# Kernel tuning notes

Hardware: AMD Instinct MI355X
Metric: run time of the kernel (lower is better)

## Reference

```python
import jax, jax.numpy as jnp
import numpy as np

NUM_HEADS = 16
HEAD_DIM = 64  # hidden 1024 / 16 heads


def setup_inputs() -> dict:
    key = jax.random.key(0)
    ks = jax.random.split(key, 4)
    B, S, D = 2, 2048, 1024
    scale = 1.0 / np.sqrt(D)
    return {
        "hidden_states": jax.random.normal(ks[0], (B, S, D), jnp.float32),
        "Wq": jax.random.normal(ks[1], (D, D), jnp.float32) * scale,
        "bq": jnp.zeros((D,), jnp.float32),
        "Wk": jax.random.normal(ks[2], (D, D), jnp.float32) * scale,
        "bk": jnp.zeros((D,), jnp.float32),
        "Wv": jax.random.normal(ks[3], (D, D), jnp.float32) * scale,
        "bv": jnp.zeros((D,), jnp.float32),
    }


def _split_heads(x):
    B, S, D = x.shape
    return x.reshape(B, S, NUM_HEADS, HEAD_DIM).transpose(0, 2, 1, 3)  # [B,H,S,dh]


def reference(hidden_states, Wq, bq, Wk, bk, Wv, bv):
    q = _split_heads(hidden_states @ Wq + bq)
    k = _split_heads(hidden_states @ Wk + bk)
    v = _split_heads(hidden_states @ Wv + bv)
    scores = jnp.einsum("bhqd,bhkd->bhqk", q, k) / jnp.sqrt(
        jnp.asarray(HEAD_DIM, hidden_states.dtype))
    probs = jax.nn.softmax(scores, axis=-1)  # dropout is identity in eval mode
    ctx = jnp.einsum("bhqk,bhkd->bhqd", probs, v)
    B, H, S, dh = ctx.shape
    return ctx.transpose(0, 2, 1, 3).reshape(B, S, H * dh)
```

## Files before the change

### kernel.cpp

```cpp
#include <hip/hip_runtime.h>
#include <hip/hip_bf16.h>


typedef __attribute__((ext_vector_type(8))) short bf16x8;
typedef __attribute__((ext_vector_type(4))) float f32x4;
typedef __attribute__((ext_vector_type(4))) int int4v;

#define MFMA16(A, B, C) __builtin_amdgcn_mfma_f32_16x16x32_bf16((A), (B), (C), 0, 0, 0)

#if __has_builtin(__builtin_amdgcn_exp2f)
#define EXP2(x) __builtin_amdgcn_exp2f(x)
#else
#define EXP2(x) exp2f(x)
#endif

static __device__ __forceinline__ unsigned short f2bf(float f) {
    union { float f; unsigned int u; } v;
    v.f = f;
    unsigned int u = v.u;
    u += ((u >> 16) & 1u) + 0x7FFFu;
    return (unsigned short)(u >> 16);
}

static __device__ __forceinline__ void gload_lds16(const void* g, void* l) {
    __builtin_amdgcn_global_load_lds(
        (const __attribute__((address_space(1))) void*)g,
        (__attribute__((address_space(3))) void*)l, 16, 0, 0);
}

__global__ __launch_bounds__(256) void cast_hs(const float* __restrict__ in,
                                               unsigned short* __restrict__ out) {
    const size_t i = ((size_t)blockIdx.x * 256 + threadIdx.x) * 8;
    float4 a0 = *reinterpret_cast<const float4*>(in + i);
    float4 a1 = *reinterpret_cast<const float4*>(in + i + 4);
    unsigned short t[8];
    t[0] = f2bf(a0.x); t[1] = f2bf(a0.y); t[2] = f2bf(a0.z); t[3] = f2bf(a0.w);
    t[4] = f2bf(a1.x); t[5] = f2bf(a1.y); t[6] = f2bf(a1.z); t[7] = f2bf(a1.w);
    *reinterpret_cast<int4v*>(out + i) = *reinterpret_cast<int4v*>(t);
}

__global__ __launch_bounds__(256) void transpose_cast_w(
    const float* __restrict__ W0, const float* __restrict__ W1,
    const float* __restrict__ W2, unsigned short* __restrict__ Wt) {
    __shared__ float Ts[64][65];
    const float* W = (blockIdx.z == 0) ? W0 : (blockIdx.z == 1) ? W1 : W2;
    unsigned short* O = Wt + (size_t)blockIdx.z * 1048576;

    const int t  = threadIdx.x;
    const int k0 = blockIdx.y * 64;
    const int n0 = blockIdx.x * 64;

    {
        const int kr = t >> 2, nc = (t & 3) * 16;
        const float* p = W + (size_t)(k0 + kr) * 1024 + n0 + nc;
        float4 r0 = *reinterpret_cast<const float4*>(p);
        float4 r1 = *reinterpret_cast<const float4*>(p + 4);
        float4 r2 = *reinterpret_cast<const float4*>(p + 8);
        float4 r3 = *reinterpret_cast<const float4*>(p + 12);
        float* d = &Ts[kr][nc];
        d[0]=r0.x; d[1]=r0.y; d[2]=r0.z; d[3]=r0.w;
        d[4]=r1.x; d[5]=r1.y; d[6]=r1.z; d[7]=r1.w;
        d[8]=r2.x; d[9]=r2.y; d[10]=r2.z; d[11]=r2.w;
        d[12]=r3.x; d[13]=r3.y; d[14]=r3.z; d[15]=r3.w;
    }
    __syncthreads();
    {
        const int nr = t >> 2, kc = (t & 3) * 16;
        unsigned short tmp[16];
#pragma unroll
        for (int i = 0; i < 16; i++) tmp[i] = f2bf(Ts[kc + i][nr]);
        unsigned short* d = O + (size_t)(n0 + nr) * 1024 + k0 + kc;
        *reinterpret_cast<int4v*>(d)     = *reinterpret_cast<int4v*>(&tmp[0]);
        *reinterpret_cast<int4v*>(d + 8) = *reinterpret_cast<int4v*>(&tmp[8]);
    }
}

__global__ __launch_bounds__(256) void qkv_gemm_dma(
    const unsigned short* __restrict__ hsb,
    const unsigned short* __restrict__ Wt,
    const float* __restrict__ b0, const float* __restrict__ b1,
    const float* __restrict__ b2,
    unsigned short* __restrict__ Qo,
    unsigned short* __restrict__ Ko,
    unsigned short* __restrict__ Vto)
{
    __shared__ unsigned short As[128][32];
    __shared__ unsigned short Bs[128][32];

    const int z = blockIdx.z;
    const unsigned short* W = Wt + (size_t)z * 1048576;
    const float* bias = (z == 0) ? b0 : (z == 1) ? b1 : b2;

    const int tid  = threadIdx.x;
    const int lane = tid & 63;
    const int w    = tid >> 6;
    const int l15  = lane & 15;
    const int quad = lane >> 4;
    const int m0   = blockIdx.y * 128;
    const int n0   = blockIdx.x * 128;
    const int wm   = (w >> 1) * 64;
    const int wn   = (w & 1) * 64;

    const int drow = lane >> 2;
    const int dcol = (lane & 3) * 8;

    f32x4 acc[4][4];
#pragma unroll
    for (int i = 0; i < 4; i++)
#pragma unroll
        for (int j = 0; j < 4; j++)
            acc[i][j] = (f32x4){0.f, 0.f, 0.f, 0.f};

    for (int k0 = 0; k0 < 1024; k0 += 32) {
        __syncthreads();
#pragma unroll
        for (int p = 0; p < 2; p++) {
            const int s = w * 2 + p;
            gload_lds16(hsb + (size_t)(m0 + s * 16 + drow) * 1024 + k0 + dcol,
                        &As[s * 16][0]);
            gload_lds16(W   + (size_t)(n0 + s * 16 + drow) * 1024 + k0 + dcol,
                        &Bs[s * 16][0]);
        }
        __syncthreads();

        bf16x8 af[4], bfr[4];
#pragma unroll
        for (int i = 0; i < 4; i++)
            af[i] = *reinterpret_cast<const bf16x8*>(&As[wm + i * 16 + l15][quad * 8]);
#pragma unroll
        for (int j = 0; j < 4; j++)
            bfr[j] = *reinterpret_cast<const bf16x8*>(&Bs[wn + j * 16 + l15][quad * 8]);
#pragma unroll
        for (int i = 0; i < 4; i++)
#pragma unroll
            for (int j = 0; j < 4; j++)
                acc[i][j] = MFMA16(af[i], bfr[j], acc[i][j]);
    }

    if (z == 0) {
        const float qs = 0.18033688f;
#pragma unroll
        for (int i = 0; i < 4; i++) {
            const int mbase = m0 + wm + i * 16 + quad * 4;
#pragma unroll
            for (int j = 0; j < 4; j++) {
                const int n = n0 + wn + j * 16 + l15;
                const int h = n >> 6, d = n & 63;
                const float bn = bias[n];
#pragma unroll
                for (int r = 0; r < 4; r++) {
                    const int mm = mbase + r;
                    const int b = mm >> 11, s = mm & 2047;
                    Qo[(((size_t)(b * 16 + h) * 2048 + s) * 64) + d] =
                        f2bf((acc[i][j][r] + bn) * qs);
                }
            }
        }
    } else if (z == 1) {
#pragma unroll
        for (int i = 0; i < 4; i++) {
            const int mbase = m0 + wm + i * 16 + quad * 4;
#pragma unroll
            for (int j = 0; j < 4; j++) {
                const int n = n0 + wn + j * 16 + l15;
                const int h = n >> 6, d = n & 63;
                const float bn = bias[n];
#pragma unroll
                for (int r = 0; r < 4; r++) {
                    const int mm = mbase + r;
                    const int b = mm >> 11, s = mm & 2047;
                    const int dsw = ((((d >> 3) ^ (s & 7)) & 7) << 3) | (d & 7);
                    Ko[(((size_t)(b * 16 + h) * 2048 + s) * 64) + dsw] =
                        f2bf(acc[i][j][r] + bn);
                }
            }
        }
    } else {
#pragma unroll
        for (int i = 0; i < 4; i++) {
            const int mbase = m0 + wm + i * 16 + quad * 4;
            const int b = mbase >> 11, s0 = mbase & 2047;
#pragma unroll
            for (int j = 0; j < 4; j++) {
                const int n = n0 + wn + j * 16 + l15;
                const int h = n >> 6, d = n & 63;
                const float bn = bias[n];
                ushort4 v4;
                v4.x = f2bf(acc[i][j][0] + bn);
                v4.y = f2bf(acc[i][j][1] + bn);
                v4.z = f2bf(acc[i][j][2] + bn);
                v4.w = f2bf(acc[i][j][3] + bn);
                const int cs  = (s0 & 63) >> 3;
                const int ssw = (s0 & ~63) | (((cs ^ (d & 7)) & 7) << 3) | (s0 & 7);
                *reinterpret_cast<ushort4*>(
                    Vto + ((size_t)(b * 16 + h) * 64 + d) * 2048 + ssw) = v4;
            }
        }
    }
}

__global__ __launch_bounds__(512) void attn3(
    const unsigned short* __restrict__ Qg,
    const unsigned short* __restrict__ Kg,
    const unsigned short* __restrict__ Vtg,
    float* __restrict__ out)
{
    __shared__ unsigned short Ks[2][64][64];
    __shared__ unsigned short Vs[2][64][64];
    __shared__ unsigned short Ps[8][16][66];

    const int tid  = threadIdx.x;
    const int lane = tid & 63;
    const int w    = tid >> 6;
    const int l15  = lane & 15;
    const int quad = lane >> 4;

    const int q0 = blockIdx.x * 128;
    const int h  = blockIdx.y;
    const int b  = blockIdx.z;
    const size_t base = (size_t)(b * 16 + h) * 2048 * 64;
    const unsigned short* Qh  = Qg  + base;
    const unsigned short* Kh  = Kg  + base;
    const unsigned short* Vth = Vtg + base;

    const int drow = lane >> 3;
    const int dcol = (lane & 7) * 8;

    bf16x8 qf[2];
#pragma unroll
    for (int ks = 0; ks < 2; ks++)
        qf[ks] = *reinterpret_cast<const bf16x8*>(
            Qh + (size_t)(q0 + w * 16 + l15) * 64 + ks * 32 + quad * 8);

    f32x4 o[4];
#pragma unroll
    for (int t = 0; t < 4; t++) o[t] = (f32x4){0.f, 0.f, 0.f, 0.f};
    float rsum[4] = {0.f, 0.f, 0.f, 0.f};

    const int c0 = (((quad + 0) ^ (l15 & 7)) & 7) * 8;
    const int c1 = (((quad + 4) ^ (l15 & 7)) & 7) * 8;

    gload_lds16(Kh  + (size_t)(w * 8 + drow) * 64 + dcol,   &Ks[0][w * 8][0]);
    gload_lds16(Vth + (size_t)(w * 8 + drow) * 2048 + dcol, &Vs[0][w * 8][0]);
    __syncthreads();

    int cur = 0;
    for (int kt = 0; kt < 32; kt++) {
        if (kt < 31) {
            const int kn = kt + 1;
            gload_lds16(Kh  + (size_t)kn * 4096 + (size_t)(w * 8 + drow) * 64 + dcol,
                        &Ks[cur ^ 1][w * 8][0]);
            gload_lds16(Vth + (size_t)(w * 8 + drow) * 2048 + kn * 64 + dcol,
                        &Vs[cur ^ 1][w * 8][0]);
        }

        const unsigned short (*Kc)[64] = Ks[cur];
        const unsigned short (*Vc)[64] = Vs[cur];

#pragma unroll
        for (int t = 0; t < 4; t++) {
            f32x4 sc = (f32x4){0.f, 0.f, 0.f, 0.f};
            {
                bf16x8 kf = *reinterpret_cast<const bf16x8*>(&Kc[t * 16 + l15][c0]);
                sc = MFMA16(qf[0], kf, sc);
            }
            {
                bf16x8 kf = *reinterpret_cast<const bf16x8*>(&Kc[t * 16 + l15][c1]);
                sc = MFMA16(qf[1], kf, sc);
            }
#pragma unroll
            for (int r = 0; r < 4; r++) {
                const float p = EXP2(sc[r]);
                rsum[r] += p;
                Ps[w][quad * 4 + r][t * 16 + l15] = f2bf(p);
            }
        }

        asm volatile("s_waitcnt lgkmcnt(0)" ::: "memory");
        __builtin_amdgcn_sched_barrier(0);

        bf16x8 pf[2];
#pragma unroll
        for (int ks = 0; ks < 2; ks++)
            pf[ks] = *reinterpret_cast<const bf16x8*>(&Ps[w][l15][ks * 32 + quad * 8]);

#pragma unroll
        for (int t = 0; t < 4; t++) {
            {
                bf16x8 vf = *reinterpret_cast<const bf16x8*>(&Vc[t * 16 + l15][c0]);
                o[t] = MFMA16(pf[0], vf, o[t]);
            }
            {
                bf16x8 vf = *reinterpret_cast<const bf16x8*>(&Vc[t * 16 + l15][c1]);
                o[t] = MFMA16(pf[1], vf, o[t]);
            }
        }

        __syncthreads();
        cur ^= 1;
    }

#pragma unroll
    for (int off = 1; off < 16; off <<= 1)
#pragma unroll
        for (int r = 0; r < 4; r++)
            rsum[r] += __shfl_xor(rsum[r], off, 64);

#pragma unroll
    for (int t = 0; t < 4; t++) {
#pragma unroll
        for (int r = 0; r < 4; r++) {
            const int q = q0 + w * 16 + quad * 4 + r;
            const size_t oidx = (((size_t)b * 2048 + q) * 16 + h) * 64 + t * 16 + l15;
            out[oidx] = o[t][r] / rsum[r];
        }
    }
}

__global__ void fill_sentinel(float* out, int n, float pat) {
    int i = blockIdx.x * blockDim.x + threadIdx.x;
    if (i < n) out[i] = pat;
}

extern "C" void kernel_launch(void* const* d_in, const int* in_sizes, int n_in,
                              void* d_out, int out_size, void* d_ws, size_t ws_size,
                              hipStream_t stream) {
    const size_t n_hs  = (size_t)4096 * 1024;
    const size_t n_w   = (size_t)1024 * 1024;
    const size_t n_qkv = n_hs;
    const size_t need = (n_hs + 3 * n_w + 3 * n_qkv) * sizeof(unsigned short);

    bool order_ok = (n_in == 7) &&
        in_sizes[0] == 4194304 &&
        in_sizes[1] == 1048576 && in_sizes[2] == 1024 &&
        in_sizes[3] == 1048576 && in_sizes[4] == 1024 &&
        in_sizes[5] == 1048576 && in_sizes[6] == 1024;
    if (!order_ok || out_size != 4194304) {
        fill_sentinel<<<(out_size + 255) / 256, 256, 0, stream>>>(
            (float*)d_out, out_size, 4.0f);
        return;
    }
    if (ws_size < need) {
        fill_sentinel<<<(out_size + 255) / 256, 256, 0, stream>>>(
            (float*)d_out, out_size, 2.0f);
        return;
    }

    const float* hs = (const float*)d_in[0];
    const float* Wq = (const float*)d_in[1];
    const float* bq = (const float*)d_in[2];
    const float* Wk = (const float*)d_in[3];
    const float* bk = (const float*)d_in[4];
    const float* Wv = (const float*)d_in[5];
    const float* bv = (const float*)d_in[6];

    unsigned short* hsb = (unsigned short*)d_ws;
    unsigned short* Wt  = hsb + n_hs;
    unsigned short* Q   = Wt + 3 * n_w;
    unsigned short* K   = Q + n_qkv;
    unsigned short* Vt  = K + n_qkv;

    cast_hs<<<2048, 256, 0, stream>>>(hs, hsb);
    transpose_cast_w<<<dim3(16, 16, 3), 256, 0, stream>>>(Wq, Wk, Wv, Wt);

    dim3 g1(8, 32, 3);
    qkv_gemm_dma<<<g1, dim3(256), 0, stream>>>(hsb, Wt, bq, bk, bv, Q, K, Vt);

    dim3 g2(16, 16, 2);
    attn3<<<g2, dim3(512), 0, stream>>>(Q, K, Vt, (float*)d_out);
}
```

Baseline: 196.9 us.

## Widen GEMM K-tile to 64, remap attention grid, repad P tile

The QKV GEMM now stages 64-wide K slices per iteration instead of 32. This halves the loop trips and barriers and issues two MFMA k-substeps per sync. The attention kernel moves to a 1D grid whose block index is decoded so that consecutive blocks come from 8 different batch-head pairs, which may change L2/cache locality of K/V. The P scratch padding changes from 66 to 68 elements to alter the LDS bank mapping. The wider A/B tiles double shared memory per GEMM block, which may reduce occupancy, and the new 64-element row stride without a swizzle may cause bank conflicts on the fragment reads.

```diff
diff --git a/kernel.cpp b/kernel.cpp
--- a/kernel.cpp
+++ b/kernel.cpp
@@ -84,8 +84,8 @@
     unsigned short* __restrict__ Ko,
     unsigned short* __restrict__ Vto)
 {
-    __shared__ unsigned short As[128][32];
-    __shared__ unsigned short Bs[128][32];
+    __shared__ unsigned short As[128][64];
+    __shared__ unsigned short Bs[128][64];
 
     const int z = blockIdx.z;
     const unsigned short* W = Wt + (size_t)z * 1048576;
@@ -101,8 +101,8 @@
     const int wm   = (w >> 1) * 64;
     const int wn   = (w & 1) * 64;
 
-    const int drow = lane >> 2;
-    const int dcol = (lane & 3) * 8;
+    const int drow = lane >> 3;
+    const int dcol = (lane & 7) * 8;
 
     f32x4 acc[4][4];
 #pragma unroll
@@ -111,30 +111,35 @@
         for (int j = 0; j < 4; j++)
             acc[i][j] = (f32x4){0.f, 0.f, 0.f, 0.f};
 
-    for (int k0 = 0; k0 < 1024; k0 += 32) {
+    for (int k0 = 0; k0 < 1024; k0 += 64) {
         __syncthreads();
 #pragma unroll
-        for (int p = 0; p < 2; p++) {
-            const int s = w * 2 + p;
-            gload_lds16(hsb + (size_t)(m0 + s * 16 + drow) * 1024 + k0 + dcol,
-                        &As[s * 16][0]);
-            gload_lds16(W   + (size_t)(n0 + s * 16 + drow) * 1024 + k0 + dcol,
-                        &Bs[s * 16][0]);
+        for (int p = 0; p < 4; p++) {
+            const int s = w * 32 + p * 8;
+            gload_lds16(hsb + (size_t)(m0 + s + drow) * 1024 + k0 + dcol,
+                        &As[s][0]);
+            gload_lds16(W   + (size_t)(n0 + s + drow) * 1024 + k0 + dcol,
+                        &Bs[s][0]);
         }
         __syncthreads();
 
-        bf16x8 af[4], bfr[4];
-#pragma unroll
-        for (int i = 0; i < 4; i++)
-            af[i] = *reinterpret_cast<const bf16x8*>(&As[wm + i * 16 + l15][quad * 8]);
-#pragma unroll
-        for (int j = 0; j < 4; j++)
-            bfr[j] = *reinterpret_cast<const bf16x8*>(&Bs[wn + j * 16 + l15][quad * 8]);
-#pragma unroll
-        for (int i = 0; i < 4; i++)
+#pragma unroll
+        for (int kk = 0; kk < 2; kk++) {
+            bf16x8 af[4], bfr[4];
+#pragma unroll
+            for (int i = 0; i < 4; i++)
+                af[i] = *reinterpret_cast<const bf16x8*>(
+                    &As[wm + i * 16 + l15][kk * 32 + quad * 8]);
 #pragma unroll
             for (int j = 0; j < 4; j++)
-                acc[i][j] = MFMA16(af[i], bfr[j], acc[i][j]);
+                bfr[j] = *reinterpret_cast<const bf16x8*>(
+                    &Bs[wn + j * 16 + l15][kk * 32 + quad * 8]);
+#pragma unroll
+            for (int i = 0; i < 4; i++)
+#pragma unroll
+                for (int j = 0; j < 4; j++)
+                    acc[i][j] = MFMA16(af[i], bfr[j], acc[i][j]);
+        }
     }
 
     if (z == 0) {
@@ -207,7 +212,7 @@
 {
     __shared__ unsigned short Ks[2][64][64];
     __shared__ unsigned short Vs[2][64][64];
-    __shared__ unsigned short Ps[8][16][66];
+    __shared__ unsigned short Ps[8][16][68];
 
     const int tid  = threadIdx.x;
     const int lane = tid & 63;
@@ -215,13 +220,16 @@
     const int l15  = lane & 15;
     const int quad = lane >> 4;
 
-    const int q0 = blockIdx.x * 128;
-    const int h  = blockIdx.y;
-    const int b  = blockIdx.z;
-    const size_t base = (size_t)(b * 16 + h) * 2048 * 64;
+    const int lin = blockIdx.x;
+    const int qb  = (lin >> 3) & 15;
+    const int bh  = (lin & 7) | ((lin >> 7) << 3);
+    const int q0  = qb * 128;
+    const size_t base = (size_t)bh * 2048 * 64;
     const unsigned short* Qh  = Qg  + base;
     const unsigned short* Kh  = Kg  + base;
     const unsigned short* Vth = Vtg + base;
+    const int b = bh >> 4;
+    const int h = bh & 15;
 
     const int drow = lane >> 3;
     const int dcol = (lane & 7) * 8;
@@ -366,6 +374,5 @@
     dim3 g1(8, 32, 3);
     qkv_gemm_dma<<<g1, dim3(256), 0, stream>>>(hsb, Wt, bq, bk, bv, Q, K, Vt);
 
-    dim3 g2(16, 16, 2);
-    attn3<<<g2, dim3(512), 0, stream>>>(Q, K, Vt, (float*)d_out);
-}
+    attn3<<<dim3(512), dim3(512), 0, stream>>>(Q, K, Vt, (float*)d_out);
+}
```

After: 196.8 us. Within noise of the previous version (-0.0%).

## Remap attention grid, pad P tile, use hardware bf16 cast, add setprio

Applied to the files above, without the earlier changes.

The attention kernel now runs on a flat 1D grid. Its block index is decoded so that blocks sharing the same batch-head land together, which is meant to improve L2 reuse of K/V across XCDs. The P staging buffer row padding grows from 66 to 68 to change LDS bank mapping. The manual float-to-bf16 rounding is replaced by the HIP intrinsic, and MFMA pairs are wrapped in s_setprio to favour matrix issue across waves. These are several independent micro-tweaks, and their combined effect on scheduling is uncertain.

```diff
diff --git a/kernel.cpp b/kernel.cpp
--- a/kernel.cpp
+++ b/kernel.cpp
@@ -20,6 +20,11 @@
     unsigned int u = v.u;
     u += ((u >> 16) & 1u) + 0x7FFFu;
     return (unsigned short)(u >> 16);
+}
+
+static __device__ __forceinline__ unsigned short f2bf_hw(float f) {
+    __hip_bfloat16 h = __float2bfloat16(f);
+    return *reinterpret_cast<unsigned short*>(&h);
 }
 
 static __device__ __forceinline__ void gload_lds16(const void* g, void* l) {
@@ -207,7 +212,7 @@
 {
     __shared__ unsigned short Ks[2][64][64];
     __shared__ unsigned short Vs[2][64][64];
-    __shared__ unsigned short Ps[8][16][66];
+    __shared__ unsigned short Ps[8][16][68];
 
     const int tid  = threadIdx.x;
     const int lane = tid & 63;
@@ -215,13 +220,16 @@
     const int l15  = lane & 15;
     const int quad = lane >> 4;
 
-    const int q0 = blockIdx.x * 128;
-    const int h  = blockIdx.y;
-    const int b  = blockIdx.z;
-    const size_t base = (size_t)(b * 16 + h) * 2048 * 64;
+    const int lin = blockIdx.x;
+    const int qb  = (lin >> 3) & 15;
+    const int bh  = (lin & 7) | ((lin >> 7) << 3);
+    const int q0  = qb * 128;
+    const size_t base = (size_t)bh * 2048 * 64;
     const unsigned short* Qh  = Qg  + base;
     const unsigned short* Kh  = Kg  + base;
     const unsigned short* Vth = Vtg + base;
+    const int b = bh >> 4;
+    const int h = bh & 15;
 
     const int drow = lane >> 3;
     const int dcol = (lane & 7) * 8;
@@ -260,19 +268,17 @@
 #pragma unroll
         for (int t = 0; t < 4; t++) {
             f32x4 sc = (f32x4){0.f, 0.f, 0.f, 0.f};
-            {
-                bf16x8 kf = *reinterpret_cast<const bf16x8*>(&Kc[t * 16 + l15][c0]);
-                sc = MFMA16(qf[0], kf, sc);
-            }
-            {
-                bf16x8 kf = *reinterpret_cast<const bf16x8*>(&Kc[t * 16 + l15][c1]);
-                sc = MFMA16(qf[1], kf, sc);
-            }
+            bf16x8 kf0 = *reinterpret_cast<const bf16x8*>(&Kc[t * 16 + l15][c0]);
+            bf16x8 kf1 = *reinterpret_cast<const bf16x8*>(&Kc[t * 16 + l15][c1]);
+            __builtin_amdgcn_s_setprio(1);
+            sc = MFMA16(qf[0], kf0, sc);
+            sc = MFMA16(qf[1], kf1, sc);
+            __builtin_amdgcn_s_setprio(0);
 #pragma unroll
             for (int r = 0; r < 4; r++) {
                 const float p = EXP2(sc[r]);
                 rsum[r] += p;
-                Ps[w][quad * 4 + r][t * 16 + l15] = f2bf(p);
+                Ps[w][quad * 4 + r][t * 16 + l15] = f2bf_hw(p);
             }
         }
 
@@ -286,14 +292,12 @@
 
 #pragma unroll
         for (int t = 0; t < 4; t++) {
-            {
-                bf16x8 vf = *reinterpret_cast<const bf16x8*>(&Vc[t * 16 + l15][c0]);
-                o[t] = MFMA16(pf[0], vf, o[t]);
-            }
-            {
-                bf16x8 vf = *reinterpret_cast<const bf16x8*>(&Vc[t * 16 + l15][c1]);
-                o[t] = MFMA16(pf[1], vf, o[t]);
-            }
+            bf16x8 vf0 = *reinterpret_cast<const bf16x8*>(&Vc[t * 16 + l15][c0]);
+            bf16x8 vf1 = *reinterpret_cast<const bf16x8*>(&Vc[t * 16 + l15][c1]);
+            __builtin_amdgcn_s_setprio(1);
+            o[t] = MFMA16(pf[0], vf0, o[t]);
+            o[t] = MFMA16(pf[1], vf1, o[t]);
+            __builtin_amdgcn_s_setprio(0);
         }
 
         __syncthreads();
@@ -366,6 +370,5 @@
     dim3 g1(8, 32, 3);
     qkv_gemm_dma<<<g1, dim3(256), 0, stream>>>(hsb, Wt, bq, bk, bv, Q, K, Vt);
 
-    dim3 g2(16, 16, 2);
-    attn3<<<g2, dim3(512), 0, stream>>>(Q, K, Vt, (float*)d_out);
-}
+    attn3<<<dim3(512), dim3(512), 0, stream>>>(Q, K, Vt, (float*)d_out);
+}
```

After: 188.2 us. 1.05x faster.
